# Optimization experiments

Measured on AMD Instinct MI355X. Metric: run time of the kernel, lower is better.

The kernel has to match this reference:

```python
import jax, jax.numpy as jnp
import numpy as np
import math

EPS = 1e-8
ROUTING_ITERS = 2
FINAL_LAMBDA = 0.01

B, O, I, D_IN, D_OUT = 64, 64, 1152, 16, 16


def setup_inputs() -> dict:
    key = jax.random.key(0)
    k1, k2, k3, k4, k5 = jax.random.split(key, 5)
    stdev = 0.2
    u = jax.random.normal(k1, (B, I, D_IN), dtype=jnp.float32)
    W = jax.random.normal(k2, (1, O, I, D_OUT, D_IN), dtype=jnp.float32) * stdev
    beta_a = jax.random.normal(k3, (1, O), dtype=jnp.float32) * stdev
    beta_u = jax.random.normal(k4, (1, O, 1, 1), dtype=jnp.float32) * stdev
    bias = jnp.full((1, O, D_OUT), 0.1, dtype=jnp.float32)
    return {"u": u, "W": W, "beta_a": beta_a, "beta_u": beta_u, "bias": bias}


def _m_step(rr, V, a_i, beta_a, beta_u, inv_temp):
    # rr: (B,O,I), V: (B,O,I,D), a_i: (B,I)
    rra = rr * a_i[:, None, :]                      # (B,O,I)
    rr_sum = jnp.sum(rra, axis=-1, keepdims=True)   # (B,O,1)
    mean_j = jnp.sum(rra[..., None] * V, axis=2) / (rr_sum + EPS)       # (B,O,D)
    diff = V - mean_j[:, :, None, :]
    var_j = jnp.sum(rra[..., None] * diff * diff, axis=2) / (rr_sum + EPS) + 1e-4  # (B,O,D)
    # beta_u broadcast: original stores (1,O,1) tiled over out_dim
    cost_j = jnp.sum((beta_u[..., 0] + jnp.log(var_j)) * rr_sum, axis=-1)  # (B,O)
    a_j = jax.nn.sigmoid(inv_temp * (beta_a - cost_j))                     # (B,O)
    return mean_j, var_j, a_j


def _e_step(mean_j, var_j, a_j, V):
    diff = V - mean_j[:, :, None, :]                                  # (B,O,I,D)
    p1 = jnp.sqrt(2.0 * math.pi * jnp.prod(var_j, axis=-1) + EPS)     # (B,O)
    log_arg = -jnp.sum(diff * diff / (2.0 * var_j[:, :, None, :] + EPS), axis=-1)  # (B,O,I)
    p_ij = jnp.exp(log_arg) / (p1[:, :, None] + EPS)                  # (B,O,I)
    ap = a_j[:, :, None] * p_ij
    rr = ap / (jnp.sum(ap, axis=1, keepdims=True) + EPS)
    return rr


def reference(u, W, beta_a, beta_u, bias):
    # votes: V[b,o,i,e] = sum_d u[b,i,d] * W[0,o,i,e,d]
    a_i = jnp.linalg.norm(u + EPS, axis=-1)                           # (B,I)
    V = jnp.einsum('bid,oied->boie', u, W[0]) + EPS + bias[:, :, None, :]  # (B,O,I,D)
    batch = u.shape[0]
    out_caps = W.shape[1]
    rr = jnp.full((batch, out_caps, V.shape[2]), 1.0 / out_caps, dtype=u.dtype)
    for i in range(ROUTING_ITERS):
        inv_temp = FINAL_LAMBDA * (1.0 - 0.95 ** (i + 1))
        mean_j, var_j, a_j = _m_step(rr, V, a_i, beta_a, beta_u, inv_temp)
        if i < ROUTING_ITERS - 1:
            rr = _e_step(mean_j, var_j, a_j, V)
    out = a_j[:, :, None] * mean_j / (jnp.linalg.norm(mean_j + EPS, axis=-1, keepdims=True) + EPS)
    return out
```

## Files before the change

kernel.cpp:

```cpp
#include <hip/hip_runtime.h>

#define EPSF 1e-8f

constexpr int NB = 64;
constexpr int NO = 64;
constexpr int NI = 1152;
constexpr int ND = 16;

constexpr int RSTRIDE = 260;
constexpr int BUFSZ   = 64 * RSTRIDE;

typedef float v2f __attribute__((ext_vector_type(2)));
typedef float v4f __attribute__((ext_vector_type(4)));

__device__ __forceinline__ void loadrow16f(const float* __restrict__ base,
                                           size_t elem, float* f){
  const float4* p = (const float4*)(base + elem);
  float4 x0=p[0], x1=p[1], x2=p[2], x3=p[3];
  f[0]=x0.x; f[1]=x0.y; f[2]=x0.z; f[3]=x0.w;
  f[4]=x1.x; f[5]=x1.y; f[6]=x1.z; f[7]=x1.w;
  f[8]=x2.x; f[9]=x2.y; f[10]=x2.z; f[11]=x2.w;
  f[12]=x3.x; f[13]=x3.y; f[14]=x3.z; f[15]=x3.w;
}

__device__ __forceinline__ void gl_lds16(const float* g, float* l){
  __builtin_amdgcn_global_load_lds(
      (const __attribute__((address_space(1))) unsigned int*)g,
      (__attribute__((address_space(3))) unsigned int*)l,
      16, 0, 0);
}

template<int NW, bool ESTEP>
__global__ __launch_bounds__(NW*64, 2) void k_heavy(
    const float* __restrict__ u, const float* __restrict__ W,
    const float* __restrict__ bias,
    const float* __restrict__ mean0, const float* __restrict__ i2v0,
    const float* __restrict__ c0,
    float* __restrict__ S1p, float* __restrict__ S2p, float* __restrict__ Wsp,
    const int CH)
{
  const int CI = NI / CH;
  constexpr int ROWS = 64 / NW;
  const int bid = blockIdx.x;
  const int bg = bid / CH, c = bid % CH;
  const int t = threadIdx.x, lane = t & 63, w = t >> 6;
  const int b0 = bg*(2*NW) + 2*w, b1 = b0 + 1;
  const int i0 = c*CI;

  __shared__ float buf[2*BUFSZ];

  float bs[16]; loadrow16f(bias, (size_t)lane*ND, bs);
  v2f mr[16], ir[16]; v2f c01 = {0.f, 0.f};
  if (ESTEP){
    const size_t m0 = ((size_t)b0*NO + lane)*ND;
    const size_t m1 = ((size_t)b1*NO + lane)*ND;
    #pragma unroll
    for (int e=0;e<16;++e){
      mr[e] = v2f{mean0[m0+e], mean0[m1+e]};
      ir[e] = v2f{i2v0[m0+e], i2v0[m1+e]};
    }
    c01 = v2f{c0[(size_t)b0*NO + lane], c0[(size_t)b1*NO + lane]};
  }

  v2f S1[16], S2[16]; v2f wsum = {0.f, 0.f};
  #pragma unroll
  for (int e=0;e<16;++e){ S1[e]=v2f{0.f,0.f}; S2[e]=v2f{0.f,0.f}; }

  auto stage = [&](int p, int i){
    const float* gbase = W + (size_t)i*256 + (size_t)lane*4;
    float* lbase = &buf[p*BUFSZ];
    #pragma unroll
    for (int r=0;r<ROWS;++r){
      const int o = w*ROWS + r;
      gl_lds16(gbase + (size_t)o*NI*256, lbase + o*RSTRIDE);
    }
  };

  int p = 0;
  stage(0, i0);

  for (int ii=0; ii<CI; ++ii){
    __syncthreads();
    if (ii+1 < CI) stage(p^1, i0+ii+1);

    const int i = i0 + ii;
    v2f u01[16];
    {
      const float4* pa = (const float4*)(u + ((size_t)b0*NI + i)*ND);
      const float4* pb = (const float4*)(u + ((size_t)b1*NI + i)*ND);
      #pragma unroll
      for (int q=0;q<4;++q){
        float4 xa = pa[q], xb = pb[q];
        u01[q*4+0] = v2f{xa.x, xb.x};
        u01[q*4+1] = v2f{xa.y, xb.y};
        u01[q*4+2] = v2f{xa.z, xb.z};
        u01[q*4+3] = v2f{xa.w, xb.w};
      }
    }
    v2f ss = {0.f, 0.f};
    #pragma unroll
    for (int d=0;d<16;++d){ v2f x = u01[d] + EPSF; ss += x*x; }
    const v2f av = {sqrtf(ss.x), sqrtf(ss.y)};

    v2f V[16];
    #pragma unroll
    for (int e=0;e<16;++e){ float b = bs[e] + EPSF; V[e] = v2f{b, b}; }
    const float* row = &buf[p*BUFSZ + lane*RSTRIDE];
    #pragma unroll
    for (int e=0;e<16;++e){
      #pragma unroll
      for (int dq=0; dq<4; ++dq){
        const float4 wv = *(const float4*)(row + e*16 + dq*4);
        const int d = dq*4;
        V[e] += wv.x*u01[d+0];
        V[e] += wv.y*u01[d+1];
        V[e] += wv.z*u01[d+2];
        V[e] += wv.w*u01[d+3];
      }
    }

    v2f wg;
    if (ESTEP){
      v2f la = {0.f, 0.f};
      #pragma unroll
      for (int e=0;e<16;++e){ v2f df = V[e]-mr[e]; la += df*df*ir[e]; }
      v2f ap = c01 * v2f{__expf(-la.x), __expf(-la.y)};
      float q0 = ap.x, q1 = ap.y;
      #pragma unroll
      for (int off=32; off; off>>=1){
        q0 += __shfl_xor(q0, off);
        q1 += __shfl_xor(q1, off);
      }
      wg = v2f{ap.x/(q0 + EPSF)*av.x, ap.y/(q1 + EPSF)*av.y};
    } else {
      wg = av;
    }
    wsum += wg;
    #pragma unroll
    for (int e=0;e<16;++e){
      v2f tv = wg*V[e]; S1[e]+=tv; S2[e]+=tv*V[e];
    }
    p ^= 1;
  }

  const size_t ba = (((size_t)b0*CH + c)*NO + lane);
  const size_t bb = (((size_t)b1*CH + c)*NO + lane);
  #pragma unroll
  for (int e=0;e<16;++e){
    S1p[ba*ND+e]=S1[e].x; S2p[ba*ND+e]=S2[e].x;
    S1p[bb*ND+e]=S1[e].y; S2p[bb*ND+e]=S2[e].y;
  }
  Wsp[ba] = wsum.x; Wsp[bb] = wsum.y;
}

__global__ __launch_bounds__(64) void k_mred(
    const float* __restrict__ beta_a, const float* __restrict__ beta_u,
    const float* __restrict__ S1p, const float* __restrict__ S2p,
    const float* __restrict__ Wsp, const int CH,
    float* __restrict__ mean0, float* __restrict__ i2v0, float* __restrict__ c0)
{
  const int bo = blockIdx.x;
  const int b = bo >> 6, o = bo & 63;
  const int t = threadIdx.x;
  const int q = t & 3, cg = t >> 2;

  v4f s1 = {0.f,0.f,0.f,0.f}, s2 = {0.f,0.f,0.f,0.f};
  for (int c = cg; c < CH; c += 16){
    const size_t base = ((((size_t)b*CH)+c)*NO + o)*ND + 4*q;
    s1 += *(const v4f*)(S1p + base);
    s2 += *(const v4f*)(S2p + base);
  }
  #pragma unroll
  for (int off=4; off<64; off<<=1){
    #pragma unroll
    for (int k=0;k<4;++k){
      s1[k] += __shfl_xor(s1[k], off);
      s2[k] += __shfl_xor(s2[k], off);
    }
  }
  float wv = 0.f;
  for (int c = t; c < CH; c += 64)
    wv += Wsp[(((size_t)b*CH)+c)*NO + o];
  #pragma unroll
  for (int off=1; off<64; off<<=1) wv += __shfl_xor(wv, off);

  const float rrsum = wv * (1.f/64.f);
  const float inv = 1.f/(rrsum + EPSF);
  const float bu = beta_u[o];
  v4f T1 = s1*(1.f/64.f), T2 = s2*(1.f/64.f);
  v4f m   = T1*inv;
  v4f var = (T2 - 2.f*m*T1 + m*m*rrsum)*inv + 1e-4f;
  v4f iv;
  float ctp = 0.f, prp = 1.f;
  #pragma unroll
  for (int k=0;k<4;++k){
    iv[k] = 1.f/(2.f*var[k] + EPSF);
    ctp += bu + __logf(var[k]);
    prp *= var[k];
  }
  ctp += __shfl_xor(ctp, 1); ctp += __shfl_xor(ctp, 2);
  prp *= __shfl_xor(prp, 1); prp *= __shfl_xor(prp, 2);

  const size_t mbase = ((size_t)b*NO + o)*ND;
  if (cg == 0){
    *(v4f*)(mean0 + mbase + 4*q) = m;
    *(v4f*)(i2v0  + mbase + 4*q) = iv;
  }
  if (t == 0){
    float cost = ctp * rrsum;
    float x  = 5.0e-4f*(beta_a[o] - cost);
    float aj = 1.f/(1.f + __expf(-x));
    float p1 = sqrtf(6.2831853071795864f*prp + EPSF);
    c0[(size_t)b*NO + o] = aj/(p1 + EPSF);
  }
}

__global__ __launch_bounds__(64) void k_final(
    const float* __restrict__ beta_a, const float* __restrict__ beta_u,
    const float* __restrict__ S1p, const float* __restrict__ S2p,
    const float* __restrict__ Wsp, const int CH,
    float* __restrict__ out)
{
  const int bo = blockIdx.x;
  const int b = bo >> 6, o = bo & 63;
  const int t = threadIdx.x;
  const int q = t & 3, cg = t >> 2;

  v4f s1 = {0.f,0.f,0.f,0.f}, s2 = {0.f,0.f,0.f,0.f};
  for (int c = cg; c < CH; c += 16){
    const size_t base = ((((size_t)b*CH)+c)*NO + o)*ND + 4*q;
    s1 += *(const v4f*)(S1p + base);
    s2 += *(const v4f*)(S2p + base);
  }
  #pragma unroll
  for (int off=4; off<64; off<<=1){
    #pragma unroll
    for (int k=0;k<4;++k){
      s1[k] += __shfl_xor(s1[k], off);
      s2[k] += __shfl_xor(s2[k], off);
    }
  }
  float wv = 0.f;
  for (int c = t; c < CH; c += 64)
    wv += Wsp[(((size_t)b*CH)+c)*NO + o];
  #pragma unroll
  for (int off=1; off<64; off<<=1) wv += __shfl_xor(wv, off);

  const float Wsum = wv;
  const float inv = 1.f/(Wsum + EPSF);
  const float bu = beta_u[o];
  v4f m   = s1*inv;
  v4f var = (s2 - 2.f*m*s1 + m*m*Wsum)*inv + 1e-4f;
  float ctp = 0.f, nrm = 0.f;
  #pragma unroll
  for (int k=0;k<4;++k){
    ctp += bu + __logf(var[k]);
    float me = m[k] + EPSF;
    nrm += me*me;
  }
  ctp += __shfl_xor(ctp, 1); ctp += __shfl_xor(ctp, 2);
  nrm += __shfl_xor(nrm, 1); nrm += __shfl_xor(nrm, 2);

  const float cost = ctp * Wsum;
  const float x  = 9.75e-4f*(beta_a[o] - cost);
  const float aj = 1.f/(1.f + __expf(-x));
  const float scale = aj/(sqrtf(nrm) + EPSF);
  if (cg == 0){
    *(v4f*)(out + (size_t)bo*ND + 4*q) = scale*m;
  }
}

extern "C" void kernel_launch(void* const* d_in, const int* in_sizes, int n_in,
                              void* d_out, int out_size, void* d_ws, size_t ws_size,
                              hipStream_t stream)
{
  const float* u      = (const float*)d_in[0];
  const float* W      = (const float*)d_in[1];
  const float* beta_a = (const float*)d_in[2];
  const float* beta_u = (const float*)d_in[3];
  const float* bias   = (const float*)d_in[4];
  float* ws  = (float*)d_ws;
  float* out = (float*)d_out;

  const size_t base_f = 2u*NB*NO*ND + NB*NO;
  auto need = [&](int ch){
    return (base_f + 2u*(size_t)NB*ch*NO*ND + (size_t)NB*ch*NO)*4;
  };
  const bool big = (ws_size >= need(64));
  const int CH = big ? 64 : 32;

  float* mean0= ws;
  float* i2v0 = mean0 + (size_t)NB*NO*ND;
  float* c0   = i2v0 + (size_t)NB*NO*ND;
  float* S1p  = c0   + (size_t)NB*NO;
  float* S2p  = S1p  + (size_t)NB*CH*NO*ND;
  float* Wsp  = S2p  + (size_t)NB*CH*NO*ND;

  if (big){
    const int GRID = (NB/16)*CH;
    k_heavy<8,false><<<GRID, 512, 0, stream>>>(u, W, bias,
                                               nullptr, nullptr, nullptr,
                                               S1p, S2p, Wsp, CH);
    k_mred<<<NB*NO, 64, 0, stream>>>(beta_a, beta_u, S1p, S2p, Wsp, CH,
                                     mean0, i2v0, c0);
    k_heavy<8,true><<<GRID, 512, 0, stream>>>(u, W, bias,
                                              mean0, i2v0, c0,
                                              S1p, S2p, Wsp, CH);
  } else {
    const int GRID = (NB/8)*CH;
    k_heavy<4,false><<<GRID, 256, 0, stream>>>(u, W, bias,
                                               nullptr, nullptr, nullptr,
                                               S1p, S2p, Wsp, CH);
    k_mred<<<NB*NO, 64, 0, stream>>>(beta_a, beta_u, S1p, S2p, Wsp, CH,
                                     mean0, i2v0, c0);
    k_heavy<4,true><<<GRID, 256, 0, stream>>>(u, W, bias,
                                              mean0, i2v0, c0,
                                              S1p, S2p, Wsp, CH);
  }
  k_final<<<NB*NO, 64, 0, stream>>>(beta_a, beta_u, S1p, S2p, Wsp, CH, out);
}
```

Before: 331.1 us.

## Add dedicated first M-step kernel and fold bias into moment reduction

Replaces the first k_heavy<...,false> pass with a specialised k_mpass kernel that accumulates bias-free vote moments (uniform rr, weights are just a_i), then adds the bias algebraically in k_mred by shifting S1/S2 using the summed weights. This drops the per-element bias add from the first pass and uses a simpler loop with a fixed 4-wave configuration. The risk is that the first pass always runs with 256-thread blocks and 8-batch groups, even when the big path is selected, which may change occupancy and W reuse relative to the previous 8-wave variant. The expanded variance formula could also behave differently numerically.

New measurement: 326.9 us (median of 2 runs). No clear change (-1.3%).

```diff
diff --git a/kernel.cpp b/kernel.cpp
--- a/kernel.cpp
+++ b/kernel.cpp
@@ -12,6 +12,7 @@
 
 typedef float v2f __attribute__((ext_vector_type(2)));
 typedef float v4f __attribute__((ext_vector_type(4)));
+
 
 __device__ __forceinline__ void loadrow16f(const float* __restrict__ base,
                                            size_t elem, float* f){
@@ -28,6 +29,90 @@
       (const __attribute__((address_space(1))) unsigned int*)g,
       (__attribute__((address_space(3))) unsigned int*)l,
       16, 0, 0);
+}
+
+__global__ __launch_bounds__(256, 2) void k_mpass(
+    const float* __restrict__ u, const float* __restrict__ W,
+    float* __restrict__ S1p, float* __restrict__ S2p, float* __restrict__ Wsp,
+    const int CH)
+{
+  const int CI = NI / CH;
+  const int bid = blockIdx.x;
+  const int bg = bid / CH, c = bid % CH;
+  const int t = threadIdx.x, lane = t & 63, w = t >> 6;
+  const int b0 = bg*8 + 2*w, b1 = b0 + 1;
+  const int i0 = c*CI;
+
+  __shared__ float buf[BUFSZ];
+
+  v2f S1[16], S2[16]; v2f wsum = {0.f, 0.f};
+  #pragma unroll
+  for (int e=0;e<16;++e){ S1[e]=v2f{0.f,0.f}; S2[e]=v2f{0.f,0.f}; }
+
+  const float* row = &buf[lane*RSTRIDE];
+
+  for (int ii=0; ii<CI; ++ii){
+    const int i = i0 + ii;
+    __syncthreads();
+    {
+      const float* g = W + (size_t)i*256 + (size_t)(w*16)*NI*256
+                         + (size_t)lane*4;
+      float* l = buf + (w*16)*RSTRIDE;
+      #pragma unroll 1
+      for (int r=0;r<16;++r){
+        gl_lds16(g, l);
+        g += (size_t)NI*256;
+        l += RSTRIDE;
+      }
+    }
+
+    v2f u01[16];
+    {
+      const float4* pa = (const float4*)(u + ((size_t)b0*NI + i)*ND);
+      const float4* pb = (const float4*)(u + ((size_t)b1*NI + i)*ND);
+      #pragma unroll
+      for (int q=0;q<4;++q){
+        float4 xa = pa[q], xb = pb[q];
+        u01[q*4+0] = v2f{xa.x, xb.x};
+        u01[q*4+1] = v2f{xa.y, xb.y};
+        u01[q*4+2] = v2f{xa.z, xb.z};
+        u01[q*4+3] = v2f{xa.w, xb.w};
+      }
+    }
+    v2f ss = {0.f, 0.f};
+    #pragma unroll
+    for (int d=0;d<16;++d){ v2f x = u01[d] + EPSF; ss += x*x; }
+    const v2f av = {sqrtf(ss.x), sqrtf(ss.y)};
+
+    __syncthreads();
+
+    #pragma unroll
+    for (int e=0;e<16;++e){
+      v2f Ve = {0.f, 0.f};
+      #pragma unroll
+      for (int dq=0; dq<4; ++dq){
+        const float4 wv = *(const float4*)(row + e*16 + dq*4);
+        const int d = dq*4;
+        Ve += wv.x*u01[d+0];
+        Ve += wv.y*u01[d+1];
+        Ve += wv.z*u01[d+2];
+        Ve += wv.w*u01[d+3];
+      }
+      v2f tv = av*Ve;
+      S1[e] += tv;
+      S2[e] += tv*Ve;
+    }
+    wsum += av;
+  }
+
+  const size_t ba = (((size_t)b0*CH + c)*NO + lane);
+  const size_t bb = (((size_t)b1*CH + c)*NO + lane);
+  #pragma unroll
+  for (int e=0;e<16;++e){
+    S1p[ba*ND+e]=S1[e].x; S2p[ba*ND+e]=S2[e].x;
+    S1p[bb*ND+e]=S1[e].y; S2p[bb*ND+e]=S2[e].y;
+  }
+  Wsp[ba] = wsum.x; Wsp[bb] = wsum.y;
 }
 
 template<int NW, bool ESTEP>
@@ -155,6 +240,7 @@
 
 __global__ __launch_bounds__(64) void k_mred(
     const float* __restrict__ beta_a, const float* __restrict__ beta_u,
+    const float* __restrict__ bias,
     const float* __restrict__ S1p, const float* __restrict__ S2p,
     const float* __restrict__ Wsp, const int CH,
     float* __restrict__ mean0, float* __restrict__ i2v0, float* __restrict__ c0)
@@ -183,6 +269,13 @@
     wv += Wsp[(((size_t)b*CH)+c)*NO + o];
   #pragma unroll
   for (int off=1; off<64; off<<=1) wv += __shfl_xor(wv, off);
+
+  {
+    v4f Bq = *(const v4f*)(bias + (size_t)o*ND + 4*q);
+    Bq += EPSF;
+    s2 += 2.f*Bq*s1 + Bq*Bq*wv;
+    s1 += Bq*wv;
+  }
 
   const float rrsum = wv * (1.f/64.f);
   const float inv = 1.f/(rrsum + EPSF);
@@ -296,26 +389,17 @@
   float* S2p  = S1p  + (size_t)NB*CH*NO*ND;
   float* Wsp  = S2p  + (size_t)NB*CH*NO*ND;
 
+  k_mpass<<<(NB/8)*CH, 256, 0, stream>>>(u, W, S1p, S2p, Wsp, CH);
+  k_mred<<<NB*NO, 64, 0, stream>>>(beta_a, beta_u, bias, S1p, S2p, Wsp, CH,
+                                   mean0, i2v0, c0);
   if (big){
-    const int GRID = (NB/16)*CH;
-    k_heavy<8,false><<<GRID, 512, 0, stream>>>(u, W, bias,
-                                               nullptr, nullptr, nullptr,
-                                               S1p, S2p, Wsp, CH);
-    k_mred<<<NB*NO, 64, 0, stream>>>(beta_a, beta_u, S1p, S2p, Wsp, CH,
-                                     mean0, i2v0, c0);
-    k_heavy<8,true><<<GRID, 512, 0, stream>>>(u, W, bias,
-                                              mean0, i2v0, c0,
-                                              S1p, S2p, Wsp, CH);
+    k_heavy<8,true><<<(NB/16)*CH, 512, 0, stream>>>(u, W, bias,
+                                                    mean0, i2v0, c0,
+                                                    S1p, S2p, Wsp, CH);
   } else {
-    const int GRID = (NB/8)*CH;
-    k_heavy<4,false><<<GRID, 256, 0, stream>>>(u, W, bias,
-                                               nullptr, nullptr, nullptr,
-                                               S1p, S2p, Wsp, CH);
-    k_mred<<<NB*NO, 64, 0, stream>>>(beta_a, beta_u, S1p, S2p, Wsp, CH,
-                                     mean0, i2v0, c0);
-    k_heavy<4,true><<<GRID, 256, 0, stream>>>(u, W, bias,
-                                              mean0, i2v0, c0,
-                                              S1p, S2p, Wsp, CH);
+    k_heavy<4,true><<<(NB/8)*CH, 256, 0, stream>>>(u, W, bias,
+                                                   mean0, i2v0, c0,
+                                                   S1p, S2p, Wsp, CH);
   }
   k_final<<<NB*NO, 64, 0, stream>>>(beta_a, beta_u, S1p, S2p, Wsp, CH, out);
 }
```

## Fuse routing phases into one cooperative kernel with grid-wide syncs

Applied to the files above, without the earlier changes.

Combines the two heavy passes and the two reduction passes into a single cooperative-launched kernel separated by grid.sync barriers, with each wave handling two (b,o) reductions. The aim is to remove the launch overhead and inter-kernel drain gaps of four separate launches. It falls back to the original multi-kernel path if the cooperative launch fails. The grid of 256 blocks at 512 threads must be co-resident, which the launch bound of two blocks per CU should allow. The cost is grid-barrier latency and a reduction phase that now runs on only 256 blocks instead of 4096.

Result: slower. 768.4 us (+132.0%).

```diff
diff --git a/kernel.cpp b/kernel.cpp
--- a/kernel.cpp
+++ b/kernel.cpp
@@ -1,4 +1,7 @@
 #include <hip/hip_runtime.h>
+#include <hip/hip_cooperative_groups.h>
+
+namespace cg = cooperative_groups;
 
 #define EPSF 1e-8f
 
@@ -12,6 +15,7 @@
 
 typedef float v2f __attribute__((ext_vector_type(2)));
 typedef float v4f __attribute__((ext_vector_type(4)));
+
 
 __device__ __forceinline__ void loadrow16f(const float* __restrict__ base,
                                            size_t elem, float* f){
@@ -31,13 +35,13 @@
 }
 
 template<int NW, bool ESTEP>
-__global__ __launch_bounds__(NW*64, 2) void k_heavy(
+__device__ __forceinline__ void heavy_phase(
     const float* __restrict__ u, const float* __restrict__ W,
     const float* __restrict__ bias,
     const float* __restrict__ mean0, const float* __restrict__ i2v0,
     const float* __restrict__ c0,
     float* __restrict__ S1p, float* __restrict__ S2p, float* __restrict__ Wsp,
-    const int CH)
+    const int CH, float* buf)
 {
   const int CI = NI / CH;
   constexpr int ROWS = 64 / NW;
@@ -46,8 +50,6 @@
   const int t = threadIdx.x, lane = t & 63, w = t >> 6;
   const int b0 = bg*(2*NW) + 2*w, b1 = b0 + 1;
   const int i0 = c*CI;
-
-  __shared__ float buf[2*BUFSZ];
 
   float bs[16]; loadrow16f(bias, (size_t)lane*ND, bs);
   v2f mr[16], ir[16]; v2f c01 = {0.f, 0.f};
@@ -153,19 +155,19 @@
   Wsp[ba] = wsum.x; Wsp[bb] = wsum.y;
 }
 
-__global__ __launch_bounds__(64) void k_mred(
+__device__ __forceinline__ void mred_wave(
+    const int lane, const int bo, const int CH,
     const float* __restrict__ beta_a, const float* __restrict__ beta_u,
     const float* __restrict__ S1p, const float* __restrict__ S2p,
-    const float* __restrict__ Wsp, const int CH,
-    float* __restrict__ mean0, float* __restrict__ i2v0, float* __restrict__ c0)
-{
-  const int bo = blockIdx.x;
+    const float* __restrict__ Wsp,
+    float* __restrict__ mean0, float* __restrict__ i2v0,
+    float* __restrict__ c0)
+{
   const int b = bo >> 6, o = bo & 63;
-  const int t = threadIdx.x;
-  const int q = t & 3, cg = t >> 2;
+  const int q = lane & 3, cgp = lane >> 2;
 
   v4f s1 = {0.f,0.f,0.f,0.f}, s2 = {0.f,0.f,0.f,0.f};
-  for (int c = cg; c < CH; c += 16){
+  for (int c = cgp; c < CH; c += 16){
     const size_t base = ((((size_t)b*CH)+c)*NO + o)*ND + 4*q;
     s1 += *(const v4f*)(S1p + base);
     s2 += *(const v4f*)(S2p + base);
@@ -179,7 +181,7 @@
     }
   }
   float wv = 0.f;
-  for (int c = t; c < CH; c += 64)
+  for (int c = lane; c < CH; c += 64)
     wv += Wsp[(((size_t)b*CH)+c)*NO + o];
   #pragma unroll
   for (int off=1; off<64; off<<=1) wv += __shfl_xor(wv, off);
@@ -202,11 +204,11 @@
   prp *= __shfl_xor(prp, 1); prp *= __shfl_xor(prp, 2);
 
   const size_t mbase = ((size_t)b*NO + o)*ND;
-  if (cg == 0){
+  if (cgp == 0){
     *(v4f*)(mean0 + mbase + 4*q) = m;
     *(v4f*)(i2v0  + mbase + 4*q) = iv;
   }
-  if (t == 0){
+  if (lane == 0){
     float cost = ctp * rrsum;
     float x  = 5.0e-4f*(beta_a[o] - cost);
     float aj = 1.f/(1.f + __expf(-x));
@@ -215,19 +217,17 @@
   }
 }
 
-__global__ __launch_bounds__(64) void k_final(
+__device__ __forceinline__ void final_wave(
+    const int lane, const int bo, const int CH,
     const float* __restrict__ beta_a, const float* __restrict__ beta_u,
     const float* __restrict__ S1p, const float* __restrict__ S2p,
-    const float* __restrict__ Wsp, const int CH,
-    float* __restrict__ out)
-{
-  const int bo = blockIdx.x;
+    const float* __restrict__ Wsp, float* __restrict__ out)
+{
   const int b = bo >> 6, o = bo & 63;
-  const int t = threadIdx.x;
-  const int q = t & 3, cg = t >> 2;
+  const int q = lane & 3, cgp = lane >> 2;
 
   v4f s1 = {0.f,0.f,0.f,0.f}, s2 = {0.f,0.f,0.f,0.f};
-  for (int c = cg; c < CH; c += 16){
+  for (int c = cgp; c < CH; c += 16){
     const size_t base = ((((size_t)b*CH)+c)*NO + o)*ND + 4*q;
     s1 += *(const v4f*)(S1p + base);
     s2 += *(const v4f*)(S2p + base);
@@ -241,7 +241,7 @@
     }
   }
   float wv = 0.f;
-  for (int c = t; c < CH; c += 64)
+  for (int c = lane; c < CH; c += 64)
     wv += Wsp[(((size_t)b*CH)+c)*NO + o];
   #pragma unroll
   for (int off=1; off<64; off<<=1) wv += __shfl_xor(wv, off);
@@ -265,9 +265,74 @@
   const float x  = 9.75e-4f*(beta_a[o] - cost);
   const float aj = 1.f/(1.f + __expf(-x));
   const float scale = aj/(sqrtf(nrm) + EPSF);
-  if (cg == 0){
+  if (cgp == 0){
     *(v4f*)(out + (size_t)bo*ND + 4*q) = scale*m;
   }
+}
+
+__global__ __launch_bounds__(512, 2) void k_fused(
+    const float* __restrict__ u, const float* __restrict__ W,
+    const float* __restrict__ beta_a, const float* __restrict__ beta_u,
+    const float* __restrict__ bias,
+    float* __restrict__ S1p, float* __restrict__ S2p, float* __restrict__ Wsp,
+    float* __restrict__ mean0, float* __restrict__ i2v0, float* __restrict__ c0,
+    float* __restrict__ out, const int CH)
+{
+  __shared__ float buf[2*BUFSZ];
+  cg::grid_group grid = cg::this_grid();
+  const int t = threadIdx.x, lane = t & 63, w = t >> 6;
+  const int wbase = ((int)blockIdx.x*8 + w)*2;
+
+  heavy_phase<8,false>(u, W, bias, nullptr, nullptr, nullptr,
+                       S1p, S2p, Wsp, CH, buf);
+  __threadfence();
+  grid.sync();
+
+  mred_wave(lane, wbase+0, CH, beta_a, beta_u, S1p, S2p, Wsp, mean0, i2v0, c0);
+  mred_wave(lane, wbase+1, CH, beta_a, beta_u, S1p, S2p, Wsp, mean0, i2v0, c0);
+  __threadfence();
+  grid.sync();
+
+  heavy_phase<8,true>(u, W, bias, mean0, i2v0, c0,
+                      S1p, S2p, Wsp, CH, buf);
+  __threadfence();
+  grid.sync();
+
+  final_wave(lane, wbase+0, CH, beta_a, beta_u, S1p, S2p, Wsp, out);
+  final_wave(lane, wbase+1, CH, beta_a, beta_u, S1p, S2p, Wsp, out);
+}
+
+template<int NW, bool ESTEP>
+__global__ __launch_bounds__(NW*64, 2) void k_heavy(
+    const float* __restrict__ u, const float* __restrict__ W,
+    const float* __restrict__ bias,
+    const float* __restrict__ mean0, const float* __restrict__ i2v0,
+    const float* __restrict__ c0,
+    float* __restrict__ S1p, float* __restrict__ S2p, float* __restrict__ Wsp,
+    const int CH)
+{
+  __shared__ float buf[2*BUFSZ];
+  heavy_phase<NW,ESTEP>(u, W, bias, mean0, i2v0, c0, S1p, S2p, Wsp, CH, buf);
+}
+
+__global__ __launch_bounds__(64) void k_mred(
+    const float* __restrict__ beta_a, const float* __restrict__ beta_u,
+    const float* __restrict__ S1p, const float* __restrict__ S2p,
+    const float* __restrict__ Wsp, const int CH,
+    float* __restrict__ mean0, float* __restrict__ i2v0, float* __restrict__ c0)
+{
+  mred_wave((int)threadIdx.x, (int)blockIdx.x, CH,
+            beta_a, beta_u, S1p, S2p, Wsp, mean0, i2v0, c0);
+}
+
+__global__ __launch_bounds__(64) void k_final(
+    const float* __restrict__ beta_a, const float* __restrict__ beta_u,
+    const float* __restrict__ S1p, const float* __restrict__ S2p,
+    const float* __restrict__ Wsp, const int CH,
+    float* __restrict__ out)
+{
+  final_wave((int)threadIdx.x, (int)blockIdx.x, CH,
+             beta_a, beta_u, S1p, S2p, Wsp, out);
 }
 
 extern "C" void kernel_launch(void* const* d_in, const int* in_sizes, int n_in,
@@ -296,26 +361,42 @@
   float* S2p  = S1p  + (size_t)NB*CH*NO*ND;
   float* Wsp  = S2p  + (size_t)NB*CH*NO*ND;
 
+  bool done = false;
   if (big){
-    const int GRID = (NB/16)*CH;
-    k_heavy<8,false><<<GRID, 512, 0, stream>>>(u, W, bias,
-                                               nullptr, nullptr, nullptr,
-                                               S1p, S2p, Wsp, CH);
-    k_mred<<<NB*NO, 64, 0, stream>>>(beta_a, beta_u, S1p, S2p, Wsp, CH,
-                                     mean0, i2v0, c0);
-    k_heavy<8,true><<<GRID, 512, 0, stream>>>(u, W, bias,
-                                              mean0, i2v0, c0,
-                                              S1p, S2p, Wsp, CH);
-  } else {
-    const int GRID = (NB/8)*CH;
-    k_heavy<4,false><<<GRID, 256, 0, stream>>>(u, W, bias,
-                                               nullptr, nullptr, nullptr,
-                                               S1p, S2p, Wsp, CH);
-    k_mred<<<NB*NO, 64, 0, stream>>>(beta_a, beta_u, S1p, S2p, Wsp, CH,
-                                     mean0, i2v0, c0);
-    k_heavy<4,true><<<GRID, 256, 0, stream>>>(u, W, bias,
-                                              mean0, i2v0, c0,
-                                              S1p, S2p, Wsp, CH);
-  }
-  k_final<<<NB*NO, 64, 0, stream>>>(beta_a, beta_u, S1p, S2p, Wsp, CH, out);
-}
+    const float *ua=u, *Wa=W, *baa=beta_a, *bua=beta_u, *bia=bias;
+    float *s1a=S1p, *s2a=S2p, *wsa=Wsp, *m0a=mean0, *iva=i2v0, *c0a=c0,
+          *oa=out;
+    int cha = CH;
+    void* args[] = {(void*)&ua, (void*)&Wa, (void*)&baa, (void*)&bua,
+                    (void*)&bia, (void*)&s1a, (void*)&s2a, (void*)&wsa,
+                    (void*)&m0a, (void*)&iva, (void*)&c0a, (void*)&oa,
+                    (void*)&cha};
+    hipError_t err = hipLaunchCooperativeKernel(
+        (const void*)k_fused, dim3((NB/16)*CH), dim3(512), args, 0, stream);
+    done = (err == hipSuccess);
+  }
+  if (!done){
+    if (big){
+      const int GRID = (NB/16)*CH;
+      k_heavy<8,false><<<GRID, 512, 0, stream>>>(u, W, bias,
+                                                 nullptr, nullptr, nullptr,
+                                                 S1p, S2p, Wsp, CH);
+      k_mred<<<NB*NO, 64, 0, stream>>>(beta_a, beta_u, S1p, S2p, Wsp, CH,
+                                       mean0, i2v0, c0);
+      k_heavy<8,true><<<GRID, 512, 0, stream>>>(u, W, bias,
+                                                mean0, i2v0, c0,
+                                                S1p, S2p, Wsp, CH);
+    } else {
+      const int GRID = (NB/8)*CH;
+      k_heavy<4,false><<<GRID, 256, 0, stream>>>(u, W, bias,
+                                                 nullptr, nullptr, nullptr,
+                                                 S1p, S2p, Wsp, CH);
+      k_mred<<<NB*NO, 64, 0, stream>>>(beta_a, beta_u, S1p, S2p, Wsp, CH,
+                                       mean0, i2v0, c0);
+      k_heavy<4,true><<<GRID, 256, 0, stream>>>(u, W, bias,
+                                                mean0, i2v0, c0,
+                                                S1p, S2p, Wsp, CH);
+    }
+    k_final<<<NB*NO, 64, 0, stream>>>(beta_a, beta_u, S1p, S2p, Wsp, CH, out);
+  }
+}
```
